# Kernel optimization log

Measured on AMD Instinct MI355X. Metric: run time of the kernel, lower is better.

## Reference

```python
import jax, jax.numpy as jnp
import numpy as np

EPS = jnp.float32(1.1920929e-07)  # torch.finfo(torch.float32).eps
LN_EPS = jnp.float32(1e-07)


def _lstm_cell(x, h, c, wih, whh, bih, bhh):
    # PyTorch gate order: i, f, g, o
    g = x @ wih.T + h @ whh.T + bih + bhh
    i, f, gg, o = jnp.split(g, 4, axis=-1)
    c2 = jax.nn.sigmoid(f) * c + jax.nn.sigmoid(i) * jnp.tanh(gg)
    h2 = jax.nn.sigmoid(o) * jnp.tanh(c2)
    return h2, c2


def _sep_block(x, state, wih1, whh1, bih1, bhh1, wih2, whh2, bih2, bhh2, dw, db):
    # x: [N, F]; state: [2, N, H, 2]  (layer, batch, hidden, h/c)
    h1, c1 = state[0, :, :, 0], state[0, :, :, 1]
    h2, c2 = state[1, :, :, 0], state[1, :, :, 1]
    h1n, c1n = _lstm_cell(x, h1, c1, wih1, whh1, bih1, bhh1)
    h2n, c2n = _lstm_cell(h1n, h2, c2, wih2, whh2, bih2, bhh2)
    mask = jax.nn.sigmoid(h2n @ dw.T + db)
    out_state = jnp.stack([jnp.stack([h1n, c1n], -1), jnp.stack([h2n, c2n], -1)], 0)
    return mask, out_state


def reference(x, in_state1, in_state2, s1_wih1, s1_whh1, s1_bih1, s1_bhh1, s1_wih2, s1_whh2, s1_bih2, s1_bhh2, s1_dw, s1_db, enc_w, ln_gamma, ln_beta, s2_wih1, s2_whh1, s2_bih1, s2_bhh1, s2_wih2, s2_whh2, s2_bih2, s2_bhh2, s2_dw, s2_db, dec_w):
    n = x.shape[-1]  # frame_len = 512
    # STFT: center=False, rect window, win_len == n_fft == input len -> one frame == rfft(x)
    y = jnp.fft.rfft(x, axis=-1)  # [N, 257]
    r, im = jnp.real(y).astype(jnp.float32), jnp.imag(y).astype(jnp.float32)
    mag = jnp.sqrt(jnp.maximum(r * r + im * im, EPS))
    phase = jnp.arctan2(im + EPS, r + EPS)
    # separation block 1 on magnitude (T=1 so LSTM is a single cell step)
    mask1, out_state1 = _sep_block(mag, in_state1, s1_wih1, s1_whh1, s1_bih1, s1_bhh1, s1_wih2, s1_whh2, s1_bih2, s1_bhh2, s1_dw, s1_db)
    est_mag = mask1 * mag
    s1_stft = est_mag * jnp.exp(phase * 1j)  # complex64 [N, 257]
    y1 = jnp.fft.irfft(s1_stft, n=n, axis=-1)  # [N, 512]
    # encoder 1x1 conv == matmul
    enc = y1 @ enc_w.T  # [N, 256]
    # instant layer norm over channel dim
    mean = jnp.mean(enc, axis=-1, keepdims=True)
    var = jnp.mean(jnp.square(enc - mean), axis=-1, keepdims=True)
    enc_n = (enc - mean) / jnp.sqrt(var + LN_EPS) * ln_gamma + ln_beta
    # separation block 2 on learned-domain features
    mask2, out_state2 = _sep_block(enc_n, in_state2, s2_wih1, s2_whh1, s2_bih1, s2_bhh1, s2_wih2, s2_whh2, s2_bih2, s2_bhh2, s2_dw, s2_db)
    decoded = (mask2 * enc) @ dec_w.T  # [N, 512]
    return decoded[:, :, None], out_state1, out_state2  # match torch [N, 512, 1]


def setup_inputs() -> dict:
    key = jax.random.key(0)
    ks = iter(jax.random.split(key, 40))
    def rn(shape, s=0.05):
        return jax.random.normal(next(ks), shape, jnp.float32) * s
    N, F, FB, H, E = 16384, 512, 257, 128, 256
    return {
        "x": rn((N, F), 1.0),
        "in_state1": rn((2, N, H, 2), 0.1),
        "in_state2": rn((2, N, H, 2), 0.1),
        "s1_wih1": rn((4 * H, FB)), "s1_whh1": rn((4 * H, H)), "s1_bih1": rn((4 * H,)), "s1_bhh1": rn((4 * H,)),
        "s1_wih2": rn((4 * H, H)), "s1_whh2": rn((4 * H, H)), "s1_bih2": rn((4 * H,)), "s1_bhh2": rn((4 * H,)),
        "s1_dw": rn((FB, H)), "s1_db": rn((FB,)),
        "enc_w": rn((E, F)),
        "ln_gamma": jnp.ones((E,), jnp.float32), "ln_beta": jnp.zeros((E,), jnp.float32),
        "s2_wih1": rn((4 * H, E)), "s2_whh1": rn((4 * H, H)), "s2_bih1": rn((4 * H,)), "s2_bhh1": rn((4 * H,)),
        "s2_wih2": rn((4 * H, H)), "s2_whh2": rn((4 * H, H)), "s2_bih2": rn((4 * H,)), "s2_bhh2": rn((4 * H,)),
        "s2_dw": rn((E, H)), "s2_db": rn((E,)),
        "dec_w": rn((F, E)),
    }
```

## Files before the change

### kernel.cpp

```cpp
#include <hip/hip_runtime.h>
#include <hip/hip_bf16.h>
#include <math.h>

static constexpr int BN   = 16384;
static constexpr int NFFT = 512;
static constexpr int NBIN = 257;
static constexpr int NH   = 128;
static constexpr int NE   = 256;
static constexpr float EPSF  = 1.1920929e-07f;
static constexpr float LNEPS = 1e-07f;

using short8  = __attribute__((ext_vector_type(8))) short;
using float4v = __attribute__((ext_vector_type(4))) float;

__device__ __forceinline__ float sigm(float x){ return 1.0f/(1.0f+expf(-x)); }
__device__ __forceinline__ ushort f2b(float v){
  __hip_bfloat16 b = __float2bfloat16(v);
  return *reinterpret_cast<ushort*>(&b);
}
__device__ __forceinline__ float b2f(ushort u){
  __hip_bfloat16 b = *reinterpret_cast<__hip_bfloat16*>(&u);
  return __bfloat162float(b);
}

__device__ __forceinline__ size_t pkoff(int rows, int row, int k, int lo){
  const int ls = ((((k >> 3) & 3) | (lo << 2)) ^ (row & 7));
  return (size_t)(k >> 5) * ((size_t)rows << 6) + ((size_t)row << 6) + (ls << 3) + (k & 7);
}
__device__ __forceinline__ void split_pk(float v, ushort* base, int rows, int row, int k){
  ushort h = f2b(v);
  base[pkoff(rows, row, k, 0)] = h;
  base[pkoff(rows, row, k, 1)] = f2b(v - b2f(h));
}
__device__ __forceinline__ float read_pk(const ushort* base, int rows, int row, int k){
  return b2f(base[pkoff(rows, row, k, 0)]) + b2f(base[pkoff(rows, row, k, 1)]);
}

__device__ __forceinline__ void gload16(const ushort* g, ushort* l){
  __builtin_amdgcn_global_load_lds(
      (const __attribute__((address_space(1))) unsigned int*)g,
      (__attribute__((address_space(3))) unsigned int*)l,
      16, 0, 0);
}

enum { M_F32 = 0, M_PLANES = 1, M_LSTM = 2, M_EST = 3, M_DEC = 4, M_RFFT = 5 };

template<int MODE>
__global__ __launch_bounds__(256)
void mfma_gemm(const ushort* __restrict__ Apk, int MA, int nkA,
               const ushort* __restrict__ Bpk, int MB,
               const ushort* __restrict__ A2pk, int nkA2,
               const ushort* __restrict__ B2pk, int MB2,
               const float* __restrict__ bias,
               float* __restrict__ C, int ldc,
               const float* __restrict__ aux0,
               const ushort* __restrict__ auxpk,
               float* __restrict__ out0,
               ushort* __restrict__ opk)
{
  constexpr int LDSW = (MODE == M_LSTM) ? 16384 : 12288;
  __shared__ ushort smem[LDSW];
  const int tid  = threadIdx.x;
  const int row0 = blockIdx.x * 64;
  const int col0 = blockIdx.y * 128;
  const int lane = tid & 63;
  const int wv   = tid >> 6;
  const int wr   = (wv >> 1) * 32;
  const int wc   = (wv & 1) * 64;
  const int fr   = lane & 15;
  const int quad = lane >> 4;

  float4v acc[2][4];
  #pragma unroll
  for (int i = 0; i < 2; ++i)
    #pragma unroll
    for (int j = 0; j < 4; ++j)
      acc[i][j] = float4v{0.f, 0.f, 0.f, 0.f};

  const int nt0 = nkA;
  const int nt1 = A2pk ? nkA2 : 0;
  const int nt  = nt0 + nt1;

  const size_t astr  = (size_t)MA << 6;
  const size_t bstr  = (size_t)MB << 6;
  const size_t bstr2 = (size_t)MB2 << 6;
  size_t abase[2], bbase[4];
  #pragma unroll
  for (int s = 0; s < 2; ++s)
    abase[s] = ((size_t)(row0 + (wv * 2 + s) * 8) << 6) + lane * 8;
  #pragma unroll
  for (int s = 0; s < 4; ++s)
    bbase[s] = ((size_t)(col0 + (wv * 4 + s) * 8) << 6) + lane * 8;

  #pragma unroll 1
  for (int t = 0; t < nt; ++t) {
    if (t < nt0) {
      #pragma unroll
      for (int s = 0; s < 2; ++s)
        gload16(Apk + (size_t)t * astr + abase[s], &smem[(wv * 2 + s) * 512]);
      #pragma unroll
      for (int s = 0; s < 4; ++s)
        gload16(Bpk + (size_t)t * bstr + bbase[s], &smem[4096 + (wv * 4 + s) * 512]);
    } else {
      const size_t kt = t - nt0;
      #pragma unroll
      for (int s = 0; s < 2; ++s)
        gload16(A2pk + kt * astr + abase[s], &smem[(wv * 2 + s) * 512]);
      #pragma unroll
      for (int s = 0; s < 4; ++s)
        gload16(B2pk + kt * bstr2 + bbase[s], &smem[4096 + (wv * 4 + s) * 512]);
    }
    asm volatile("s_waitcnt vmcnt(0)" ::: "memory");
    __syncthreads();

    const char* Ab = (const char*)smem;
    const char* Bb = (const char*)(smem + 4096);
    short8 ah[2], al[2], bh[4], bl[4];
    #pragma unroll
    for (int i = 0; i < 2; ++i) {
      const int ra  = wr + i * 16 + fr;
      const int swa = (ra & 7) << 4;
      ah[i] = *(const short8*)(Ab + ra * 128 + ((quad << 4) ^ swa));
      al[i] = *(const short8*)(Ab + ra * 128 + ((64 | (quad << 4)) ^ swa));
    }
    #pragma unroll
    for (int j = 0; j < 4; ++j) {
      const int rb  = wc + j * 16 + fr;
      const int swb = (rb & 7) << 4;
      bh[j] = *(const short8*)(Bb + rb * 128 + ((quad << 4) ^ swb));
      bl[j] = *(const short8*)(Bb + rb * 128 + ((64 | (quad << 4)) ^ swb));
    }
    #pragma unroll
    for (int i = 0; i < 2; ++i)
      #pragma unroll
      for (int j = 0; j < 4; ++j) {
        acc[i][j] = __builtin_amdgcn_mfma_f32_16x16x32_bf16(ah[i], bh[j], acc[i][j], 0, 0, 0);
        acc[i][j] = __builtin_amdgcn_mfma_f32_16x16x32_bf16(ah[i], bl[j], acc[i][j], 0, 0, 0);
        acc[i][j] = __builtin_amdgcn_mfma_f32_16x16x32_bf16(al[i], bh[j], acc[i][j], 0, 0, 0);
      }
    __syncthreads();
  }

  if constexpr (MODE == M_F32) {
    #pragma unroll
    for (int j = 0; j < 4; ++j) {
      const int colb = col0 + wc + j * 16 + fr;
      const float bv = bias ? bias[colb] : 0.f;
      #pragma unroll
      for (int i = 0; i < 2; ++i)
        #pragma unroll
        for (int r = 0; r < 4; ++r) {
          const int row = row0 + wr + i * 16 + quad * 4 + r;
          C[(size_t)row * ldc + colb] = acc[i][j][r] + bv;
        }
    }
  } else if constexpr (MODE == M_PLANES) {
    #pragma unroll
    for (int j = 0; j < 4; ++j) {
      const int colb = col0 + wc + j * 16 + fr;
      #pragma unroll
      for (int i = 0; i < 2; ++i)
        #pragma unroll
        for (int r = 0; r < 4; ++r) {
          const int row = row0 + wr + i * 16 + quad * 4 + r;
          split_pk(acc[i][j][r], opk, ldc, row, colb);
        }
    }
  } else if constexpr (MODE == M_RFFT) {
    #pragma unroll
    for (int j = 0; j < 4; ++j) {
      const int colb = col0 + wc + j * 16 + fr;
      #pragma unroll
      for (int i = 0; i < 2; ++i)
        #pragma unroll
        for (int r = 0; r < 4; ++r) {
          const int row = row0 + wr + i * 16 + quad * 4 + r;
          const float v = acc[i][j][r];
          C[(size_t)row * ldc + colb] = v;
          const float w = __shfl_xor(v, 1, 64);
          if (!(lane & 1)) {
            const int bin = colb >> 1;
            const float mg = sqrtf(fmaxf(v * v + w * w, EPSF));
            split_pk(mg, opk, BN, row, bin);
          }
        }
    }
  } else if constexpr (MODE == M_EST) {
    #pragma unroll
    for (int j = 0; j < 4; ++j) {
      const int colg = col0 + wc + j * 16 + fr;
      const float bv = bias[colg];
      #pragma unroll
      for (int i = 0; i < 2; ++i)
        #pragma unroll
        for (int r = 0; r < 4; ++r) {
          const int row = row0 + wr + i * 16 + quad * 4 + r;
          if (colg < NBIN) {
            const float m   = sigm(acc[i][j][r] + bv);
            const float mag = read_pk(auxpk, BN, row, colg);
            const float e   = m * mag;
            const float rr  = aux0[(size_t)row * 514 + 2 * colg];
            const float im  = aux0[(size_t)row * 514 + 2 * colg + 1];
            const float re = rr + EPSF, ie = im + EPSF;
            const float hyp = fmaxf(sqrtf(re * re + ie * ie), 1e-35f);
            split_pk(e * re / hyp, opk, BN, row, 2 * colg);
            split_pk(e * ie / hyp, opk, BN, row, 2 * colg + 1);
          } else if (colg < 272) {
            const int k0 = 2 * colg;
            opk[pkoff(BN, row, k0, 0)] = 0;     opk[pkoff(BN, row, k0, 1)] = 0;
            opk[pkoff(BN, row, k0 + 1, 0)] = 0; opk[pkoff(BN, row, k0 + 1, 1)] = 0;
          }
        }
    }
  } else if constexpr (MODE == M_DEC) {
    #pragma unroll
    for (int j = 0; j < 4; ++j) {
      const int colg = col0 + wc + j * 16 + fr;
      const float bv = bias[colg];
      #pragma unroll
      for (int i = 0; i < 2; ++i)
        #pragma unroll
        for (int r = 0; r < 4; ++r) {
          const int row = row0 + wr + i * 16 + quad * 4 + r;
          const float v = sigm(acc[i][j][r] + bv) * aux0[(size_t)row * NE + colg];
          split_pk(v, opk, BN, row, colg);
        }
    }
  } else {
    float* Ep = (float*)smem;
    const int ub = blockIdx.y << 5;
    #pragma unroll
    for (int j = 0; j < 4; ++j) {
      const int cl = wc + j * 16 + fr;
      const float bv = bias[col0 + cl];
      #pragma unroll
      for (int i = 0; i < 2; ++i)
        #pragma unroll
        for (int r = 0; r < 4; ++r)
          Ep[(wr + i * 16 + quad * 4 + r) * 128 + cl] = acc[i][j][r] + bv;
    }
    __syncthreads();
    #pragma unroll
    for (int k = 0; k < 8; ++k) {
      const int cell = tid + 256 * k;
      const int ul = cell & 31;
      const int er = cell >> 5;
      const int row = row0 + er;
      const int unit = ub + ul;
      const float gi = Ep[er * 128 + ul];
      const float gf = Ep[er * 128 + 32 + ul];
      const float gc = Ep[er * 128 + 64 + ul];
      const float go = Ep[er * 128 + 96 + ul];
      const size_t sidx = (size_t)row * NH + unit;
      const float cp = aux0[2 * sidx + 1];
      const float cn = sigm(gf) * cp + sigm(gi) * tanhf(gc);
      const float hn = sigm(go) * tanhf(cn);
      split_pk(hn, opk, BN, row, unit);
      float2 hc; hc.x = hn; hc.y = cn;
      *(float2*)(out0 + 2 * sidx) = hc;
    }
  }
}

__device__ __forceinline__ void do_wconv_pk(const float* src, int M0, int K0,
                                            ushort* dst, int Mp, int Kp, int li){
  int r = li / Kp, k = li - r * Kp;
  float v = (r < M0 && k < K0) ? src[(size_t)r * K0 + k] : 0.f;
  split_pk(v, dst, Mp, r, k);
}
__device__ __forceinline__ void do_wconv_g_pk(const float* src, int K0,
                                              ushort* dst, int Kp, int li){
  int rp = li / Kp, k = li - rp * Kp;
  int y = rp >> 7, g = (rp >> 5) & 3, u = (y << 5) | (rp & 31);
  float v = (k < K0) ? src[(size_t)(g * 128 + u) * K0 + k] : 0.f;
  split_pk(v, dst, 512, rp, k);
}

__global__ void prep_all(
    const float* s1_wih1, const float* s1_whh1, const float* s1_wih2,
    const float* s1_whh2, const float* s1_dw,   const float* enc_w,
    const float* s2_wih1, const float* s2_whh1, const float* s2_wih2,
    const float* s2_whh2, const float* s2_dw,   const float* dec_w,
    const float* s1_bih1, const float* s1_bhh1, const float* s1_bih2,
    const float* s1_bhh2, const float* s1_db,
    const float* s2_bih1, const float* s2_bhh1, const float* s2_bih2,
    const float* s2_bhh2, const float* s2_db,
    ushort* fwdTpk, ushort* invTtpk,
    ushort* w11pk, ushort* wh1pk, ushort* w12pk, ushort* wh2pk,
    ushort* dw1pk, ushort* encwpk, ushort* w21pk, ushort* wh3pk,
    ushort* w22pk, ushort* wh4pk, ushort* dw2pk, ushort* decwpk,
    float* bg1, float* bg2, float* bm1, float* bg3, float* bg4, float* bm2)
{
  int idx = blockIdx.x * blockDim.x + threadIdx.x;
  if (idx < 262144) {
    int c = idx >> 9, n = idx & 511;
    int k = c >> 1, m = (k * n) & 511;
    float th = (float)m * (6.283185307179586f / 512.0f);
    float s, co; sincosf(th, &s, &co);
    split_pk((c & 1) ? -s : co, fwdTpk, 512, c, n);
  } else if (idx < 589824) {
    int li = idx - 262144;
    int c = li >> 9, n = li & 511;
    float v = 0.f;
    if (c < 512) {
      int k = c >> 1, m = (k * n) & 511;
      float th = (float)m * (6.283185307179586f / 512.0f);
      float s, co; sincosf(th, &s, &co);
      float w = (k == 0) ? (1.0f / 512.0f) : (2.0f / 512.0f);
      v = (c & 1) ? -w * s : w * co;
    } else if (c == 512) {
      v = ((n & 1) ? -1.0f : 1.0f) / 512.0f;
    }
    split_pk(v, invTtpk, 640, c, n);
  } else if (idx < 737280)  { do_wconv_g_pk(s1_wih1, 257, w11pk, 288, idx - 589824);
  } else if (idx < 802816)  { do_wconv_g_pk(s1_whh1, 128, wh1pk, 128, idx - 737280);
  } else if (idx < 868352)  { do_wconv_g_pk(s1_wih2, 128, w12pk, 128, idx - 802816);
  } else if (idx < 933888)  { do_wconv_g_pk(s1_whh2, 128, wh2pk, 128, idx - 868352);
  } else if (idx < 983040)  { do_wconv_pk(s1_dw, 257, 128, dw1pk, 384, 128, idx - 933888);
  } else if (idx < 1114112) { do_wconv_pk(enc_w, 256, 512, encwpk, 256, 512, idx - 983040);
  } else if (idx < 1245184) { do_wconv_g_pk(s2_wih1, 256, w21pk, 256, idx - 1114112);
  } else if (idx < 1310720) { do_wconv_g_pk(s2_whh1, 128, wh3pk, 128, idx - 1245184);
  } else if (idx < 1376256) { do_wconv_g_pk(s2_wih2, 128, w22pk, 128, idx - 1310720);
  } else if (idx < 1441792) { do_wconv_g_pk(s2_whh2, 128, wh4pk, 128, idx - 1376256);
  } else if (idx < 1474560) { do_wconv_pk(s2_dw, 256, 128, dw2pk, 256, 128, idx - 1441792);
  } else if (idx < 1605632) { do_wconv_pk(dec_w, 512, 256, decwpk, 512, 256, idx - 1474560);
  } else if (idx < 1606144) {
    int rp = idx - 1605632;
    int y = rp >> 7, g = (rp >> 5) & 3, u = (y << 5) | (rp & 31);
    int sr = g * 128 + u;
    bg1[rp] = s1_bih1[sr] + s1_bhh1[sr];
  } else if (idx < 1606656) {
    int rp = idx - 1606144;
    int y = rp >> 7, g = (rp >> 5) & 3, u = (y << 5) | (rp & 31);
    int sr = g * 128 + u;
    bg2[rp] = s1_bih2[sr] + s1_bhh2[sr];
  } else if (idx < 1607040) {
    int i = idx - 1606656;
    bm1[i] = (i < 257) ? s1_db[i] : 0.f;
  } else if (idx < 1607552) {
    int rp = idx - 1607040;
    int y = rp >> 7, g = (rp >> 5) & 3, u = (y << 5) | (rp & 31);
    int sr = g * 128 + u;
    bg3[rp] = s2_bih1[sr] + s2_bhh1[sr];
  } else if (idx < 1608064) {
    int rp = idx - 1607552;
    int y = rp >> 7, g = (rp >> 5) & 3, u = (y << 5) | (rp & 31);
    int sr = g * 128 + u;
    bg4[rp] = s2_bih2[sr] + s2_bhh2[sr];
  } else if (idx < 1608320) {
    int i = idx - 1608064;
    bm2[i] = s2_db[i];
  }
}

__global__ __launch_bounds__(256)
void input_prep(const float* __restrict__ x, ushort* __restrict__ XSpk,
                const float* __restrict__ st1,
                ushort* __restrict__ h1pk, ushort* __restrict__ h2pk,
                const float* __restrict__ st2,
                ushort* __restrict__ h3pk, ushort* __restrict__ h4pk,
                float* __restrict__ RI, ushort* __restrict__ magpk)
{
  __shared__ float L[16 * 516];
  const int tid = threadIdx.x;
  const int b   = blockIdx.x;
  if (b < BN / 16) {
    const int row0 = b * 16;
    #pragma unroll
    for (int i = 0; i < 8; ++i) {
      int g = i * 1024 + tid * 4;
      int row = g >> 9, col = g & 511;
      *(float4v*)&L[row * 516 + col] = *(const float4v*)(x + (size_t)row0 * 512 + g);
    }
    __syncthreads();
    if (tid < 128) {
      int row = tid >> 3, seg = tid & 7;
      const float* Lr = &L[row * 516 + seg * 64];
      float s = 0.f;
      #pragma unroll
      for (int i = 0; i < 64; i += 4) {
        float4v v4 = *(const float4v*)(Lr + i);
        s += (v4[0] - v4[1]) + (v4[2] - v4[3]);
      }
      s += __shfl_xor(s, 1, 64);
      s += __shfl_xor(s, 2, 64);
      s += __shfl_xor(s, 4, 64);
      if (seg == 0) {
        int grow = row0 + row;
        RI[(size_t)grow * 514 + 512] = s;
        RI[(size_t)grow * 514 + 513] = 0.f;
        split_pk(sqrtf(fmaxf(s * s, EPSF)), magpk, BN, grow, 256);
      }
    }
    #pragma unroll 1
    for (int u = tid; u < 16 * 31; u += 256) {
      int row = row0 + (u / 31), bin = 257 + (u % 31);
      magpk[pkoff(BN, row, bin, 0)] = 0;
      magpk[pkoff(BN, row, bin, 1)] = 0;
    }
    #pragma unroll
    for (int i = 0; i < 8; ++i) {
      int u = i * 256 + tid;
      int kt = u >> 7, unit = u & 127;
      int row = unit >> 3, pslot = unit & 7;
      int ls = pslot ^ (row & 7);
      const float* src = &L[row * 516 + kt * 32 + (ls & 3) * 8];
      float4v a = *(const float4v*)(src);
      float4v c = *(const float4v*)(src + 4);
      short8 out;
      if (ls < 4) {
        #pragma unroll
        for (int e = 0; e < 4; ++e) out[e]     = (short)f2b(a[e]);
        #pragma unroll
        for (int e = 0; e < 4; ++e) out[4 + e] = (short)f2b(c[e]);
      } else {
        #pragma unroll
        for (int e = 0; e < 4; ++e) {
          ushort h = f2b(a[e]);
          out[e] = (short)f2b(a[e] - b2f(h));
        }
        #pragma unroll
        for (int e = 0; e < 4; ++e) {
          ushort h = f2b(c[e]);
          out[4 + e] = (short)f2b(c[e] - b2f(h));
        }
      }
      *(short8*)(XSpk + (size_t)kt * ((size_t)BN << 6) +
                 ((size_t)(row0 + row) << 6) + pslot * 8) = out;
    }
    if (tid < 128) {
      int row = tid >> 3, pslot = tid & 7;
      short8 z;
      #pragma unroll
      for (int e = 0; e < 8; ++e) z[e] = 0;
      *(short8*)(XSpk + (size_t)16 * ((size_t)BN << 6) +
                 ((size_t)(row0 + row) << 6) + pslot * 8) = z;
    }
  } else {
    const int lb    = b - BN / 16;
    const int layer = lb >> 10;
    const int row0  = (lb & 1023) * 16;
    const float* st = (layer < 2) ? st1 : st2;
    const float* sp = st + ((layer & 1) ? (size_t)BN * NH * 2 : 0) +
                      (size_t)row0 * 256;
    ushort* hp = (layer == 0) ? h1pk : (layer == 1) ? h2pk :
                 (layer == 2) ? h3pk : h4pk;
    #pragma unroll
    for (int i = 0; i < 4; ++i) {
      int g = i * 1024 + tid * 4;
      int row = g >> 8, col = g & 255;
      *(float4v*)&L[row * 260 + col] = *(const float4v*)(sp + g);
    }
    __syncthreads();
    #pragma unroll
    for (int it = 0; it < 2; ++it) {
      int u = it * 256 + tid;
      int kt = u >> 7, unit = u & 127;
      int row = unit >> 3, pslot = unit & 7;
      int ls = pslot ^ (row & 7);
      const float* src = &L[row * 260 + (kt * 32 + (ls & 3) * 8) * 2];
      float4v v0 = *(const float4v*)(src);
      float4v v1 = *(const float4v*)(src + 4);
      float4v v2 = *(const float4v*)(src + 8);
      float4v v3 = *(const float4v*)(src + 12);
      float hvals[8] = { v0[0], v0[2], v1[0], v1[2], v2[0], v2[2], v3[0], v3[2] };
      short8 out;
      if (ls < 4) {
        #pragma unroll
        for (int e = 0; e < 8; ++e) out[e] = (short)f2b(hvals[e]);
      } else {
        #pragma unroll
        for (int e = 0; e < 8; ++e) {
          ushort h = f2b(hvals[e]);
          out[e] = (short)f2b(hvals[e] - b2f(h));
        }
      }
      *(short8*)(hp + (size_t)kt * ((size_t)BN << 6) +
                 ((size_t)(row0 + row) << 6) + pslot * 8) = out;
    }
  }
}

__global__ void ln_kernel(const float* __restrict__ ENC,
                          const float* __restrict__ gamma,
                          const float* __restrict__ beta,
                          ushort* __restrict__ opk){
  int row = blockIdx.x;
  int t = threadIdx.x;
  const float* e = ENC + (size_t)row * NE;
  float v[4]; float s = 0.f;
  #pragma unroll
  for (int i = 0; i < 4; ++i) { v[i] = e[4 * t + i]; s += v[i]; }
  #pragma unroll
  for (int off = 32; off >= 1; off >>= 1) s += __shfl_xor(s, off, 64);
  float mean = s * (1.0f / NE);
  float d[4]; float ss = 0.f;
  #pragma unroll
  for (int i = 0; i < 4; ++i) { d[i] = v[i] - mean; ss += d[i] * d[i]; }
  #pragma unroll
  for (int off = 32; off >= 1; off >>= 1) ss += __shfl_xor(ss, off, 64);
  float inv = 1.0f / sqrtf(ss * (1.0f / NE) + LNEPS);
  #pragma unroll
  for (int i = 0; i < 4; ++i) {
    int col = 4 * t + i;
    float o = d[i] * inv * gamma[col] + beta[col];
    split_pk(o, opk, BN, row, col);
  }
}

extern "C" void kernel_launch(void* const* d_in, const int* in_sizes, int n_in,
                              void* d_out, int out_size, void* d_ws, size_t ws_size,
                              hipStream_t stream)
{
  const float* x       = (const float*)d_in[0];
  const float* st1     = (const float*)d_in[1];
  const float* st2     = (const float*)d_in[2];
  const float* s1_wih1 = (const float*)d_in[3];
  const float* s1_whh1 = (const float*)d_in[4];
  const float* s1_bih1 = (const float*)d_in[5];
  const float* s1_bhh1 = (const float*)d_in[6];
  const float* s1_wih2 = (const float*)d_in[7];
  const float* s1_whh2 = (const float*)d_in[8];
  const float* s1_bih2 = (const float*)d_in[9];
  const float* s1_bhh2 = (const float*)d_in[10];
  const float* s1_dw   = (const float*)d_in[11];
  const float* s1_db   = (const float*)d_in[12];
  const float* enc_w   = (const float*)d_in[13];
  const float* ln_g    = (const float*)d_in[14];
  const float* ln_b    = (const float*)d_in[15];
  const float* s2_wih1 = (const float*)d_in[16];
  const float* s2_whh1 = (const float*)d_in[17];
  const float* s2_bih1 = (const float*)d_in[18];
  const float* s2_bhh1 = (const float*)d_in[19];
  const float* s2_wih2 = (const float*)d_in[20];
  const float* s2_whh2 = (const float*)d_in[21];
  const float* s2_bih2 = (const float*)d_in[22];
  const float* s2_bhh2 = (const float*)d_in[23];
  const float* s2_dw   = (const float*)d_in[24];
  const float* s2_db   = (const float*)d_in[25];
  const float* dec_w   = (const float*)d_in[26];

  float* out_dec = (float*)d_out;
  float* out_st1 = out_dec + (size_t)BN * NFFT;
  float* out_st2 = out_st1 + (size_t)2 * BN * NH * 2;

  char* base = (char*)d_ws;
  size_t off = 0;
  auto alloc = [&](size_t bytes) -> void* {
    off = (off + 255) & ~(size_t)255;
    void* p = base + off;
    off += bytes;
    return p;
  };
  auto pkbytes = [](int rows, int nk) -> size_t {
    return (size_t)nk * rows * 64 * 2;
  };
  ushort* fwdTpk  = (ushort*)alloc(pkbytes(512, 16));
  ushort* invTtpk = (ushort*)alloc(pkbytes(640, 16));
  ushort* MEpk    = (ushort*)alloc(pkbytes(256, 20));
  ushort* XSpk    = (ushort*)alloc(pkbytes(BN, 17));
  float*  RI      = (float*) alloc((size_t)BN * 514 * 4);
  ushort* magpk   = (ushort*)alloc(pkbytes(BN, 9));
  float*  ENC     = (float*) alloc((size_t)BN * NE * 4);
  ushort* ENCNpk  = (ushort*)alloc(pkbytes(BN, 8));
  ushort* Dpk     = (ushort*)alloc(pkbytes(BN, 8));
  ushort* h1pk    = (ushort*)alloc(pkbytes(BN, 4));
  ushort* h2pk    = (ushort*)alloc(pkbytes(BN, 4));
  ushort* h3pk    = (ushort*)alloc(pkbytes(BN, 4));
  ushort* h4pk    = (ushort*)alloc(pkbytes(BN, 4));
  ushort* h1npk   = (ushort*)alloc(pkbytes(BN, 4));
  ushort* h2npk   = (ushort*)alloc(pkbytes(BN, 4));
  ushort* w11pk   = (ushort*)alloc(pkbytes(512, 9));
  ushort* wh1pk   = (ushort*)alloc(pkbytes(512, 4));
  ushort* w12pk   = (ushort*)alloc(pkbytes(512, 4));
  ushort* wh2pk   = (ushort*)alloc(pkbytes(512, 4));
  ushort* dw1pk   = (ushort*)alloc(pkbytes(384, 4));
  ushort* encwpk  = (ushort*)alloc(pkbytes(256, 16));
  ushort* w21pk   = (ushort*)alloc(pkbytes(512, 8));
  ushort* wh3pk   = (ushort*)alloc(pkbytes(512, 4));
  ushort* w22pk   = (ushort*)alloc(pkbytes(512, 4));
  ushort* wh4pk   = (ushort*)alloc(pkbytes(512, 4));
  ushort* dw2pk   = (ushort*)alloc(pkbytes(256, 4));
  ushort* decwpk  = (ushort*)alloc(pkbytes(512, 8));
  float* bg1 = (float*)alloc(512*4); float* bg2 = (float*)alloc(512*4);
  float* bm1 = (float*)alloc(384*4);
  float* bg3 = (float*)alloc(512*4); float* bg4 = (float*)alloc(512*4);
  float* bm2 = (float*)alloc(256*4);
  (void)ws_size; (void)in_sizes; (void)n_in; (void)out_size;

  const dim3 blk(256);

  prep_all<<<(1608320 + 255) / 256, blk, 0, stream>>>(
      s1_wih1, s1_whh1, s1_wih2, s1_whh2, s1_dw, enc_w,
      s2_wih1, s2_whh1, s2_wih2, s2_whh2, s2_dw, dec_w,
      s1_bih1, s1_bhh1, s1_bih2, s1_bhh2, s1_db,
      s2_bih1, s2_bhh1, s2_bih2, s2_bhh2, s2_db,
      fwdTpk, invTtpk,
      w11pk, wh1pk, w12pk, wh2pk, dw1pk, encwpk, w21pk, wh3pk,
      w22pk, wh4pk, dw2pk, decwpk,
      bg1, bg2, bm1, bg3, bg4, bm2);

  mfma_gemm<M_PLANES><<<dim3(4,5), blk, 0, stream>>>(encwpk, 256, 16, invTtpk, 640,
      nullptr, 0, nullptr, 0,
      nullptr, nullptr, 256, nullptr, nullptr, nullptr, MEpk);

  input_prep<<<BN / 16 + 4 * (BN / 16), blk, 0, stream>>>(
      x, XSpk, st1, h1pk, h2pk, st2, h3pk, h4pk, RI, magpk);

  mfma_gemm<M_RFFT><<<dim3(256,4), blk, 0, stream>>>(XSpk, BN, 16, fwdTpk, 512,
      nullptr, 0, nullptr, 0,
      nullptr, RI, 514, nullptr, nullptr, nullptr, magpk);

  mfma_gemm<M_LSTM><<<dim3(256,4), blk, 0, stream>>>(magpk, BN, 9, w11pk, 512,
      h1pk, 4, wh1pk, 512,
      bg1, nullptr, 0, st1, nullptr, out_st1, h1npk);
  mfma_gemm<M_LSTM><<<dim3(256,4), blk, 0, stream>>>(h1npk, BN, 4, w12pk, 512,
      h2pk, 4, wh2pk, 512,
      bg2, nullptr, 0, st1 + (size_t)BN*NH*2, nullptr,
      out_st1 + (size_t)BN*NH*2, h2npk);
  mfma_gemm<M_EST><<<dim3(256,3), blk, 0, stream>>>(h2npk, BN, 4, dw1pk, 384,
      nullptr, 0, nullptr, 0,
      bm1, nullptr, 0, RI, magpk, nullptr, XSpk);

  mfma_gemm<M_F32><<<dim3(256,2), blk, 0, stream>>>(XSpk, BN, 17, MEpk, 256,
      nullptr, 0, nullptr, 0,
      nullptr, ENC, 256, nullptr, nullptr, nullptr, nullptr);
  ln_kernel<<<BN, 64, 0, stream>>>(ENC, ln_g, ln_b, ENCNpk);

  mfma_gemm<M_LSTM><<<dim3(256,4), blk, 0, stream>>>(ENCNpk, BN, 8, w21pk, 512,
      h3pk, 4, wh3pk, 512,
      bg3, nullptr, 0, st2, nullptr, out_st2, h1npk);
  mfma_gemm<M_LSTM><<<dim3(256,4), blk, 0, stream>>>(h1npk, BN, 4, w22pk, 512,
      h4pk, 4, wh4pk, 512,
      bg4, nullptr, 0, st2 + (size_t)BN*NH*2, nullptr,
      out_st2 + (size_t)BN*NH*2, h2npk);
  mfma_gemm<M_DEC><<<dim3(256,2), blk, 0, stream>>>(h2npk, BN, 4, dw2pk, 256,
      nullptr, 0, nullptr, 0,
      bm2, nullptr, 0, ENC, nullptr, nullptr, Dpk);

  mfma_gemm<M_F32><<<dim3(256,4), blk, 0, stream>>>(Dpk, BN, 8, decwpk, 512,
      nullptr, 0, nullptr, 0,
      nullptr, out_dec, 512, nullptr, nullptr, nullptr, nullptr);
}
```

Baseline: 315.8 us.

## Retile GEMMs to 32-row blocks covering the full output width

Restructures the MFMA GEMM template so each block handles 32 rows and the entire N dimension, with one wave per 64 output columns, instead of a 64x128 tile on a 2D grid. The A tile is loaded once per block and reused across all columns, which cuts redundant reads of the large activation matrices. The LSTM epilogue now has every gate for a row in LDS, so one block finishes all hidden units. The cost is larger LDS footprints and blocks of up to 640 threads, which may lower occupancy, while B tiles are reloaded by more blocks.

```diff
diff --git a/kernel.cpp b/kernel.cpp
--- a/kernel.cpp
+++ b/kernel.cpp
@@ -45,8 +45,8 @@
 
 enum { M_F32 = 0, M_PLANES = 1, M_LSTM = 2, M_EST = 3, M_DEC = 4, M_RFFT = 5 };
 
-template<int MODE>
-__global__ __launch_bounds__(256)
+template<int MODE, int WAVES>
+__global__ __launch_bounds__(WAVES * 64)
 void mfma_gemm(const ushort* __restrict__ Apk, int MA, int nkA,
                const ushort* __restrict__ Bpk, int MB,
                const ushort* __restrict__ A2pk, int nkA2,
@@ -58,15 +58,14 @@
                float* __restrict__ out0,
                ushort* __restrict__ opk)
 {
-  constexpr int LDSW = (MODE == M_LSTM) ? 16384 : 12288;
-  __shared__ ushort smem[LDSW];
+  constexpr int NT   = WAVES * 64;
+  constexpr int LDSU = 2048 + WAVES * 64 * 64;
+  __shared__ ushort smem[LDSU];
   const int tid  = threadIdx.x;
-  const int row0 = blockIdx.x * 64;
-  const int col0 = blockIdx.y * 128;
+  const int row0 = blockIdx.x * 32;
   const int lane = tid & 63;
   const int wv   = tid >> 6;
-  const int wr   = (wv >> 1) * 32;
-  const int wc   = (wv & 1) * 64;
+  const int wc   = wv * 64;
   const int fr   = lane & 15;
   const int quad = lane >> 4;
 
@@ -84,41 +83,31 @@
   const size_t astr  = (size_t)MA << 6;
   const size_t bstr  = (size_t)MB << 6;
   const size_t bstr2 = (size_t)MB2 << 6;
-  size_t abase[2], bbase[4];
-  #pragma unroll
-  for (int s = 0; s < 2; ++s)
-    abase[s] = ((size_t)(row0 + (wv * 2 + s) * 8) << 6) + lane * 8;
-  #pragma unroll
-  for (int s = 0; s < 4; ++s)
-    bbase[s] = ((size_t)(col0 + (wv * 4 + s) * 8) << 6) + lane * 8;
+  constexpr int NSEG = 4 + WAVES * 8;
 
   #pragma unroll 1
   for (int t = 0; t < nt; ++t) {
-    if (t < nt0) {
-      #pragma unroll
-      for (int s = 0; s < 2; ++s)
-        gload16(Apk + (size_t)t * astr + abase[s], &smem[(wv * 2 + s) * 512]);
-      #pragma unroll
-      for (int s = 0; s < 4; ++s)
-        gload16(Bpk + (size_t)t * bstr + bbase[s], &smem[4096 + (wv * 4 + s) * 512]);
-    } else {
-      const size_t kt = t - nt0;
-      #pragma unroll
-      for (int s = 0; s < 2; ++s)
-        gload16(A2pk + kt * astr + abase[s], &smem[(wv * 2 + s) * 512]);
-      #pragma unroll
-      for (int s = 0; s < 4; ++s)
-        gload16(B2pk + kt * bstr2 + bbase[s], &smem[4096 + (wv * 4 + s) * 512]);
+    const ushort* Ap = (t < nt0) ? (Apk + (size_t)t * astr)
+                                 : (A2pk + (size_t)(t - nt0) * astr);
+    const ushort* Bp = (t < nt0) ? (Bpk + (size_t)t * bstr)
+                                 : (B2pk + (size_t)(t - nt0) * bstr2);
+    #pragma unroll 1
+    for (int s = wv; s < NSEG; s += WAVES) {
+      if (s < 4)
+        gload16(Ap + ((size_t)(row0 + s * 8) << 6) + lane * 8, &smem[s * 512]);
+      else
+        gload16(Bp + ((size_t)((s - 4) * 8) << 6) + lane * 8,
+                &smem[2048 + (s - 4) * 512]);
     }
     asm volatile("s_waitcnt vmcnt(0)" ::: "memory");
     __syncthreads();
 
     const char* Ab = (const char*)smem;
-    const char* Bb = (const char*)(smem + 4096);
+    const char* Bb = (const char*)(smem + 2048);
     short8 ah[2], al[2], bh[4], bl[4];
     #pragma unroll
     for (int i = 0; i < 2; ++i) {
-      const int ra  = wr + i * 16 + fr;
+      const int ra  = i * 16 + fr;
       const int swa = (ra & 7) << 4;
       ah[i] = *(const short8*)(Ab + ra * 128 + ((quad << 4) ^ swa));
       al[i] = *(const short8*)(Ab + ra * 128 + ((64 | (quad << 4)) ^ swa));
@@ -144,37 +133,37 @@
   if constexpr (MODE == M_F32) {
     #pragma unroll
     for (int j = 0; j < 4; ++j) {
-      const int colb = col0 + wc + j * 16 + fr;
+      const int colb = wc + j * 16 + fr;
       const float bv = bias ? bias[colb] : 0.f;
       #pragma unroll
       for (int i = 0; i < 2; ++i)
         #pragma unroll
         for (int r = 0; r < 4; ++r) {
-          const int row = row0 + wr + i * 16 + quad * 4 + r;
+          const int row = row0 + i * 16 + quad * 4 + r;
           C[(size_t)row * ldc + colb] = acc[i][j][r] + bv;
         }
     }
   } else if constexpr (MODE == M_PLANES) {
     #pragma unroll
     for (int j = 0; j < 4; ++j) {
-      const int colb = col0 + wc + j * 16 + fr;
+      const int colb = wc + j * 16 + fr;
       #pragma unroll
       for (int i = 0; i < 2; ++i)
         #pragma unroll
         for (int r = 0; r < 4; ++r) {
-          const int row = row0 + wr + i * 16 + quad * 4 + r;
+          const int row = row0 + i * 16 + quad * 4 + r;
           split_pk(acc[i][j][r], opk, ldc, row, colb);
         }
     }
   } else if constexpr (MODE == M_RFFT) {
     #pragma unroll
     for (int j = 0; j < 4; ++j) {
-      const int colb = col0 + wc + j * 16 + fr;
+      const int colb = wc + j * 16 + fr;
       #pragma unroll
       for (int i = 0; i < 2; ++i)
         #pragma unroll
         for (int r = 0; r < 4; ++r) {
-          const int row = row0 + wr + i * 16 + quad * 4 + r;
+          const int row = row0 + i * 16 + quad * 4 + r;
           const float v = acc[i][j][r];
           C[(size_t)row * ldc + colb] = v;
           const float w = __shfl_xor(v, 1, 64);
@@ -188,13 +177,13 @@
   } else if constexpr (MODE == M_EST) {
     #pragma unroll
     for (int j = 0; j < 4; ++j) {
-      const int colg = col0 + wc + j * 16 + fr;
+      const int colg = wc + j * 16 + fr;
       const float bv = bias[colg];
       #pragma unroll
       for (int i = 0; i < 2; ++i)
         #pragma unroll
         for (int r = 0; r < 4; ++r) {
-          const int row = row0 + wr + i * 16 + quad * 4 + r;
+          const int row = row0 + i * 16 + quad * 4 + r;
           if (colg < NBIN) {
             const float m   = sigm(acc[i][j][r] + bv);
             const float mag = read_pk(auxpk, BN, row, colg);
@@ -215,42 +204,41 @@
   } else if constexpr (MODE == M_DEC) {
     #pragma unroll
     for (int j = 0; j < 4; ++j) {
-      const int colg = col0 + wc + j * 16 + fr;
+      const int colg = wc + j * 16 + fr;
       const float bv = bias[colg];
       #pragma unroll
       for (int i = 0; i < 2; ++i)
         #pragma unroll
         for (int r = 0; r < 4; ++r) {
-          const int row = row0 + wr + i * 16 + quad * 4 + r;
+          const int row = row0 + i * 16 + quad * 4 + r;
           const float v = sigm(acc[i][j][r] + bv) * aux0[(size_t)row * NE + colg];
           split_pk(v, opk, BN, row, colg);
         }
     }
   } else {
     float* Ep = (float*)smem;
-    const int ub = blockIdx.y << 5;
     #pragma unroll
     for (int j = 0; j < 4; ++j) {
       const int cl = wc + j * 16 + fr;
-      const float bv = bias[col0 + cl];
+      const float bv = bias[cl];
       #pragma unroll
       for (int i = 0; i < 2; ++i)
         #pragma unroll
         for (int r = 0; r < 4; ++r)
-          Ep[(wr + i * 16 + quad * 4 + r) * 128 + cl] = acc[i][j][r] + bv;
+          Ep[(i * 16 + quad * 4 + r) * 512 + cl] = acc[i][j][r] + bv;
     }
     __syncthreads();
     #pragma unroll
-    for (int k = 0; k < 8; ++k) {
-      const int cell = tid + 256 * k;
-      const int ul = cell & 31;
-      const int er = cell >> 5;
-      const int row = row0 + er;
-      const int unit = ub + ul;
-      const float gi = Ep[er * 128 + ul];
-      const float gf = Ep[er * 128 + 32 + ul];
-      const float gc = Ep[er * 128 + 64 + ul];
-      const float go = Ep[er * 128 + 96 + ul];
+    for (int k = 0; k < 4096 / NT; ++k) {
+      const int cell = tid + NT * k;
+      const int rin  = cell >> 7;
+      const int unit = cell & 127;
+      const float* g = Ep + rin * 512 + ((unit >> 5) << 7) + (unit & 31);
+      const float gi = g[0];
+      const float gf = g[32];
+      const float gc = g[64];
+      const float go = g[96];
+      const int row = row0 + rin;
       const size_t sidx = (size_t)row * NH + unit;
       const float cp = aux0[2 * sidx + 1];
       const float cn = sigm(gf) * cp + sigm(gi) * tanhf(gc);
@@ -600,45 +588,45 @@
       w22pk, wh4pk, dw2pk, decwpk,
       bg1, bg2, bm1, bg3, bg4, bm2);
 
-  mfma_gemm<M_PLANES><<<dim3(4,5), blk, 0, stream>>>(encwpk, 256, 16, invTtpk, 640,
+  mfma_gemm<M_PLANES, 10><<<8, 640, 0, stream>>>(encwpk, 256, 16, invTtpk, 640,
       nullptr, 0, nullptr, 0,
       nullptr, nullptr, 256, nullptr, nullptr, nullptr, MEpk);
 
   input_prep<<<BN / 16 + 4 * (BN / 16), blk, 0, stream>>>(
       x, XSpk, st1, h1pk, h2pk, st2, h3pk, h4pk, RI, magpk);
 
-  mfma_gemm<M_RFFT><<<dim3(256,4), blk, 0, stream>>>(XSpk, BN, 16, fwdTpk, 512,
+  mfma_gemm<M_RFFT, 8><<<BN / 32, 512, 0, stream>>>(XSpk, BN, 16, fwdTpk, 512,
       nullptr, 0, nullptr, 0,
       nullptr, RI, 514, nullptr, nullptr, nullptr, magpk);
 
-  mfma_gemm<M_LSTM><<<dim3(256,4), blk, 0, stream>>>(magpk, BN, 9, w11pk, 512,
+  mfma_gemm<M_LSTM, 8><<<BN / 32, 512, 0, stream>>>(magpk, BN, 9, w11pk, 512,
       h1pk, 4, wh1pk, 512,
       bg1, nullptr, 0, st1, nullptr, out_st1, h1npk);
-  mfma_gemm<M_LSTM><<<dim3(256,4), blk, 0, stream>>>(h1npk, BN, 4, w12pk, 512,
+  mfma_gemm<M_LSTM, 8><<<BN / 32, 512, 0, stream>>>(h1npk, BN, 4, w12pk, 512,
       h2pk, 4, wh2pk, 512,
       bg2, nullptr, 0, st1 + (size_t)BN*NH*2, nullptr,
       out_st1 + (size_t)BN*NH*2, h2npk);
-  mfma_gemm<M_EST><<<dim3(256,3), blk, 0, stream>>>(h2npk, BN, 4, dw1pk, 384,
+  mfma_gemm<M_EST, 6><<<BN / 32, 384, 0, stream>>>(h2npk, BN, 4, dw1pk, 384,
       nullptr, 0, nullptr, 0,
       bm1, nullptr, 0, RI, magpk, nullptr, XSpk);
 
-  mfma_gemm<M_F32><<<dim3(256,2), blk, 0, stream>>>(XSpk, BN, 17, MEpk, 256,
+  mfma_gemm<M_F32, 4><<<BN / 32, 256, 0, stream>>>(XSpk, BN, 17, MEpk, 256,
       nullptr, 0, nullptr, 0,
       nullptr, ENC, 256, nullptr, nullptr, nullptr, nullptr);
   ln_kernel<<<BN, 64, 0, stream>>>(ENC, ln_g, ln_b, ENCNpk);
 
-  mfma_gemm<M_LSTM><<<dim3(256,4), blk, 0, stream>>>(ENCNpk, BN, 8, w21pk, 512,
+  mfma_gemm<M_LSTM, 8><<<BN / 32, 512, 0, stream>>>(ENCNpk, BN, 8, w21pk, 512,
       h3pk, 4, wh3pk, 512,
       bg3, nullptr, 0, st2, nullptr, out_st2, h1npk);
-  mfma_gemm<M_LSTM><<<dim3(256,4), blk, 0, stream>>>(h1npk, BN, 4, w22pk, 512,
+  mfma_gemm<M_LSTM, 8><<<BN / 32, 512, 0, stream>>>(h1npk, BN, 4, w22pk, 512,
       h4pk, 4, wh4pk, 512,
       bg4, nullptr, 0, st2 + (size_t)BN*NH*2, nullptr,
       out_st2 + (size_t)BN*NH*2, h2npk);
-  mfma_gemm<M_DEC><<<dim3(256,2), blk, 0, stream>>>(h2npk, BN, 4, dw2pk, 256,
+  mfma_gemm<M_DEC, 4><<<BN / 32, 256, 0, stream>>>(h2npk, BN, 4, dw2pk, 256,
       nullptr, 0, nullptr, 0,
       bm2, nullptr, 0, ENC, nullptr, nullptr, Dpk);
 
-  mfma_gemm<M_F32><<<dim3(256,4), blk, 0, stream>>>(Dpk, BN, 8, decwpk, 512,
+  mfma_gemm<M_F32, 8><<<BN / 32, 512, 0, stream>>>(Dpk, BN, 8, decwpk, 512,
       nullptr, 0, nullptr, 0,
       nullptr, out_dec, 512, nullptr, nullptr, nullptr, nullptr);
 }
```

Measured after the change: 386.6 us. 1.22x slower.
